# Kernel tuning notes

Hardware: AMD Instinct MI355X
Metric: run time of the kernel (lower is better)

## Reference

```python
import jax, jax.numpy as jnp
import numpy as np

H, T, D = 16, 4096, 64
N_SEQ = 8  # packed sequences -> cu_seqlens has N_SEQ+1 entries


def setup_inputs() -> dict:
    key = jax.random.key(0)
    kq, kk, kv, kc = jax.random.split(key, 4)
    q = jax.random.normal(kq, (1, H, T, D), dtype=jnp.float32)
    k = jax.random.normal(kk, (1, H, T, D), dtype=jnp.float32)
    v = jax.random.normal(kv, (1, H, T, D), dtype=jnp.float32)
    # cu_seqlens: monotonically increasing offsets, starts at 0, ends at T
    interior = jnp.sort(jax.random.randint(kc, (N_SEQ - 1,), 1, T, dtype=jnp.int32))
    cu_seqlens = jnp.concatenate([
        jnp.zeros((1,), jnp.int32), interior, jnp.full((1,), T, jnp.int32)
    ])
    return {"q": q, "k": k, "v": v, "cu_seqlens": cu_seqlens}


def reference(q, k, v, cu_seqlens):
    # Faithful to flash_attn_varlen_func(..., causal=False) on packed sequences:
    # non-causal attention restricted block-diagonally to each segment.
    scale = 1.0 / jnp.sqrt(jnp.asarray(D, q.dtype))
    # segment id for every token position
    pos = jnp.arange(T)
    seg = jnp.searchsorted(cu_seqlens[1:], pos, side="right")  # [T]
    mask = seg[:, None] == seg[None, :]                         # [T, T] block-diagonal
    # scores: [1, H, T, T]
    scores = jnp.einsum("bhqd,bhkd->bhqk", q, k) * scale
    neg = jnp.asarray(jnp.finfo(scores.dtype).min, scores.dtype)
    scores = jnp.where(mask[None, None], scores, neg)
    attn = jax.nn.softmax(scores, axis=-1)
    out = jnp.einsum("bhqk,bhkd->bhqd", attn, v)  # [1, H, T, D]
    return out
```

## Files before the change

### kernel.cpp

```cpp
#include <hip/hip_runtime.h>

#define HH 16
#define TT 4096
#define DD 64

typedef __attribute__((ext_vector_type(2))) __fp16 half2r;
typedef __attribute__((ext_vector_type(4))) _Float16 half4;
typedef __attribute__((ext_vector_type(8))) _Float16 half8;
typedef __attribute__((ext_vector_type(4))) float float4v;

__global__ __launch_bounds__(256, 4) void pa_fwd(
    const float* __restrict__ qg, const float* __restrict__ kg,
    const float* __restrict__ vg, const int* __restrict__ cu,
    float* __restrict__ outg)
{
    __shared__ __align__(16) _Float16 Kl[2][64 * 64];
    __shared__ __align__(16) _Float16 Vl[2][64 * 64];

    const int tid  = threadIdx.x;
    const int lane = tid & 63;
    const int wave = tid >> 6;
    const int lr   = lane & 15;
    const int lg   = lane >> 4;

    const int bswz = ((int)blockIdx.x & 7) * 128 + ((int)blockIdx.x >> 3);
    const int h    = bswz >> 6;
    const int qblk = (bswz & 63) << 6;
    const int q    = qblk + wave * 16 + lr;

    int s = 0;
    while (cu[s + 1] <= q) ++s;
    const int lo = cu[s], hi = cu[s + 1];

    int sb = 0;
    while (cu[sb + 1] <= qblk) ++sb;
    const int blo = cu[sb];
    while (cu[sb + 1] <= qblk + 63) ++sb;
    const int bhi = cu[sb + 1];

    const int wlo = __shfl(lo, 0);
    const int whi = __shfl(hi, 15);
    const int mlo = __shfl(lo, 15);
    const int mhi = __shfl(hi, 0);

    const float qscale = 0.125f * 1.44269504088896f;
    const float* qrow = qg + ((size_t)h * TT + q) * DD;
    half8 qf8[2];
#pragma unroll
    for (int ds = 0; ds < 2; ++ds) {
        const float* qp = qrow + ds * 32 + lg * 8;
        float4v a = *(const float4v*)qp;
        float4v b = *(const float4v*)(qp + 4);
        half2r p0 = __builtin_amdgcn_cvt_pkrtz(a[0] * qscale, a[1] * qscale);
        half2r p1 = __builtin_amdgcn_cvt_pkrtz(a[2] * qscale, a[3] * qscale);
        half2r p2 = __builtin_amdgcn_cvt_pkrtz(b[0] * qscale, b[1] * qscale);
        half2r p3 = __builtin_amdgcn_cvt_pkrtz(b[2] * qscale, b[3] * qscale);
        qf8[ds][0] = (_Float16)p0[0]; qf8[ds][1] = (_Float16)p0[1];
        qf8[ds][2] = (_Float16)p1[0]; qf8[ds][3] = (_Float16)p1[1];
        qf8[ds][4] = (_Float16)p2[0]; qf8[ds][5] = (_Float16)p2[1];
        qf8[ds][6] = (_Float16)p3[0]; qf8[ds][7] = (_Float16)p3[1];
    }

    const float* kh_ = kg + (size_t)h * TT * DD;
    const float* vh_ = vg + (size_t)h * TT * DD;

    const int srow = tid >> 2;
    const int sc   = tid & 3;
    const unsigned kwrA = (unsigned)(srow * 128 + (((2 * sc)     ^ (srow & 7)) << 4));
    const unsigned kwrB = (unsigned)(srow * 128 + (((2 * sc + 1) ^ (srow & 7)) << 4));
    const int vd2 = tid & 31;
    const int vko = tid >> 5;
    const int vslot = vko ^ (vd2 & 7);
    const int vhb   = (vd2 >> 3) & 1;
    const unsigned vwA0 = (unsigned)(vd2 * 128 + vslot * 16 + 8 * vhb);
    const unsigned vwA1 = (unsigned)(vd2 * 128 + vslot * 16 + 8 * (1 ^ vhb));
    const unsigned vwB0 = vwA0 + 32 * 128;
    const unsigned vwB1 = vwA1 + 32 * 128;

    const unsigned kb0 = (unsigned)(lr * 128 + (((lg)     ^ (lr & 7)) << 4));
    const unsigned kb1 = (unsigned)(lr * 128 + (((4 + lg) ^ (lr & 7)) << 4));
    unsigned vrb[4];
#pragma unroll
    for (int t = 0; t < 4; ++t)
        vrb[t] = (unsigned)(lr * 128 + (((2 * t + (lg >> 1)) ^ (lr & 7)) << 4) +
                            (((lg & 1) ^ ((lr >> 3) & 1)) << 3));

    half4 onesv;
    onesv[0] = onesv[1] = onesv[2] = onesv[3] = (_Float16)1.0f;

    float4v kq[4];
    float vvA[8], vvB[8];
    const int t0k = blo & ~63;
    const float4v* kp = (const float4v*)(kh_ + (size_t)(t0k + srow) * DD + sc * 16);
    const float*   vp = vh_ + (size_t)(t0k + vko * 8) * DD + vd2;

#define ISSUE()                                                                \
    {                                                                          \
        kq[0] = kp[0]; kq[1] = kp[1]; kq[2] = kp[2]; kq[3] = kp[3];            \
        kp += (64 * DD) / 4;                                                   \
        _Pragma("unroll")                                                      \
        for (int c = 0; c < 8; ++c) {                                          \
            vvA[c] = vp[c * DD];                                               \
            vvB[c] = vp[c * DD + 32];                                          \
        }                                                                      \
        vp += 64 * DD;                                                         \
    }

    ISSUE();

    float4v acc[4];
#pragma unroll
    for (int dt = 0; dt < 4; ++dt) acc[dt] = (float4v){0.f, 0.f, 0.f, 0.f};
    float4v acc_l = (float4v){0.f, 0.f, 0.f, 0.f};
    float m_run = -1e30f;

    int cur = 0;
    for (int kt = t0k; kt < bhi; kt += 64) {
        {
            char* Kb = (char*)Kl[cur];
            char* Vb = (char*)Vl[cur];
            half8 hk0, hk1;
#pragma unroll
            for (int i = 0; i < 2; ++i) {
                half2r a = __builtin_amdgcn_cvt_pkrtz(kq[i][0], kq[i][1]);
                half2r b = __builtin_amdgcn_cvt_pkrtz(kq[i][2], kq[i][3]);
                hk0[4 * i + 0] = (_Float16)a[0]; hk0[4 * i + 1] = (_Float16)a[1];
                hk0[4 * i + 2] = (_Float16)b[0]; hk0[4 * i + 3] = (_Float16)b[1];
                half2r c2 = __builtin_amdgcn_cvt_pkrtz(kq[2 + i][0], kq[2 + i][1]);
                half2r d2 = __builtin_amdgcn_cvt_pkrtz(kq[2 + i][2], kq[2 + i][3]);
                hk1[4 * i + 0] = (_Float16)c2[0]; hk1[4 * i + 1] = (_Float16)c2[1];
                hk1[4 * i + 2] = (_Float16)d2[0]; hk1[4 * i + 3] = (_Float16)d2[1];
            }
            *(half8*)(Kb + kwrA) = hk0;
            *(half8*)(Kb + kwrB) = hk1;

            half4 uA0, uA1, uB0, uB1;
            {
                half2r a = __builtin_amdgcn_cvt_pkrtz(vvA[0], vvA[1]);
                half2r b = __builtin_amdgcn_cvt_pkrtz(vvA[2], vvA[3]);
                uA0[0] = (_Float16)a[0]; uA0[1] = (_Float16)a[1];
                uA0[2] = (_Float16)b[0]; uA0[3] = (_Float16)b[1];
                half2r c2 = __builtin_amdgcn_cvt_pkrtz(vvA[4], vvA[5]);
                half2r d2 = __builtin_amdgcn_cvt_pkrtz(vvA[6], vvA[7]);
                uA1[0] = (_Float16)c2[0]; uA1[1] = (_Float16)c2[1];
                uA1[2] = (_Float16)d2[0]; uA1[3] = (_Float16)d2[1];
                half2r e = __builtin_amdgcn_cvt_pkrtz(vvB[0], vvB[1]);
                half2r f = __builtin_amdgcn_cvt_pkrtz(vvB[2], vvB[3]);
                uB0[0] = (_Float16)e[0]; uB0[1] = (_Float16)e[1];
                uB0[2] = (_Float16)f[0]; uB0[3] = (_Float16)f[1];
                half2r g = __builtin_amdgcn_cvt_pkrtz(vvB[4], vvB[5]);
                half2r k2 = __builtin_amdgcn_cvt_pkrtz(vvB[6], vvB[7]);
                uB1[0] = (_Float16)g[0]; uB1[1] = (_Float16)g[1];
                uB1[2] = (_Float16)k2[0]; uB1[3] = (_Float16)k2[1];
            }
            *(half4*)(Vb + vwA0) = uA0;
            *(half4*)(Vb + vwA1) = uA1;
            *(half4*)(Vb + vwB0) = uB0;
            *(half4*)(Vb + vwB1) = uB1;
        }
        __syncthreads();

        if (kt + 64 < bhi) ISSUE();

        if (!(kt + 64 <= wlo || kt >= whi)) {
            const char* Kb = (const char*)Kl[cur];
            const char* Vb = (const char*)Vl[cur];

            float st[4][4];
            const bool fullv = (kt >= mlo) && (kt + 64 <= mhi);
            __builtin_amdgcn_s_setprio(1);
#pragma unroll
            for (int t = 0; t < 4; ++t) {
                float4v sa = (float4v){0.f, 0.f, 0.f, 0.f};
                half8 kf0 = *(const half8*)(Kb + kb0 + t * 2048);
                half8 kf1 = *(const half8*)(Kb + kb1 + t * 2048);
                sa = __builtin_amdgcn_mfma_f32_16x16x32_f16(kf0, qf8[0], sa, 0, 0, 0);
                sa = __builtin_amdgcn_mfma_f32_16x16x32_f16(kf1, qf8[1], sa, 0, 0, 0);
                if (fullv) {
#pragma unroll
                    for (int j = 0; j < 4; ++j) st[t][j] = sa[j];
                } else {
#pragma unroll
                    for (int j = 0; j < 4; ++j) {
                        const int key = kt + t * 16 + lg * 4 + j;
                        st[t][j] = (key >= lo && key < hi) ? sa[j] : -1e30f;
                    }
                }
            }
            __builtin_amdgcn_s_setprio(0);

            half4 vf01[2][4];
#pragma unroll
            for (int t = 0; t < 2; ++t)
#pragma unroll
                for (int dt = 0; dt < 4; ++dt)
                    vf01[t][dt] = *(const half4*)(Vb + vrb[t] + dt * 2048);

            float lmax = fmaxf(fmaxf(st[0][0], st[0][1]), fmaxf(st[0][2], st[0][3]));
            lmax = fmaxf(lmax, fmaxf(fmaxf(st[1][0], st[1][1]), fmaxf(st[1][2], st[1][3])));
            lmax = fmaxf(lmax, fmaxf(fmaxf(st[2][0], st[2][1]), fmaxf(st[2][2], st[2][3])));
            lmax = fmaxf(lmax, fmaxf(fmaxf(st[3][0], st[3][1]), fmaxf(st[3][2], st[3][3])));

            if (__any(lmax > m_run + 11.54f)) {
                float tx = fmaxf(lmax, __shfl_xor(lmax, 16));
                tx = fmaxf(tx, __shfl_xor(tx, 32));
                const float mn = fmaxf(m_run, tx);
                const float a  = exp2f(m_run - mn);
#pragma unroll
                for (int dt = 0; dt < 4; ++dt)
#pragma unroll
                    for (int j = 0; j < 4; ++j) acc[dt][j] *= a;
#pragma unroll
                for (int j = 0; j < 4; ++j) acc_l[j] *= a;
                m_run = mn;
            }

            half4 pb[4];
#pragma unroll
            for (int t = 0; t < 4; ++t) {
                float e0 = exp2f(st[t][0] - m_run);
                float e1 = exp2f(st[t][1] - m_run);
                float e2 = exp2f(st[t][2] - m_run);
                float e3 = exp2f(st[t][3] - m_run);
                half2r a = __builtin_amdgcn_cvt_pkrtz(e0, e1);
                half2r b = __builtin_amdgcn_cvt_pkrtz(e2, e3);
                pb[t][0] = (_Float16)a[0]; pb[t][1] = (_Float16)a[1];
                pb[t][2] = (_Float16)b[0]; pb[t][3] = (_Float16)b[1];
            }

            __builtin_amdgcn_s_setprio(1);
#pragma unroll
            for (int t = 0; t < 2; ++t) {
#pragma unroll
                for (int dt = 0; dt < 4; ++dt)
                    acc[dt] = __builtin_amdgcn_mfma_f32_16x16x16f16(vf01[t][dt], pb[t], acc[dt], 0, 0, 0);
                acc_l = __builtin_amdgcn_mfma_f32_16x16x16f16(onesv, pb[t], acc_l, 0, 0, 0);
            }
#pragma unroll
            for (int t = 2; t < 4; ++t) {
#pragma unroll
                for (int dt = 0; dt < 4; ++dt) {
                    half4 vf = *(const half4*)(Vb + vrb[t] + dt * 2048);
                    acc[dt] = __builtin_amdgcn_mfma_f32_16x16x16f16(vf, pb[t], acc[dt], 0, 0, 0);
                }
                acc_l = __builtin_amdgcn_mfma_f32_16x16x16f16(onesv, pb[t], acc_l, 0, 0, 0);
            }
            __builtin_amdgcn_s_setprio(0);
        }
        cur ^= 1;
    }

    const float inv = 1.0f / acc_l[0];
    float* orow = outg + ((size_t)h * TT + q) * DD;
#pragma unroll
    for (int dt = 0; dt < 4; ++dt) {
        float4v o;
#pragma unroll
        for (int j = 0; j < 4; ++j) o[j] = acc[dt][j] * inv;
        *(float4v*)(orow + dt * 16 + lg * 4) = o;
    }
#undef ISSUE
}

extern "C" void kernel_launch(void* const* d_in, const int* in_sizes, int n_in,
                              void* d_out, int out_size, void* d_ws, size_t ws_size,
                              hipStream_t stream) {
    const float* q  = (const float*)d_in[0];
    const float* k  = (const float*)d_in[1];
    const float* v  = (const float*)d_in[2];
    const int*   cu = (const int*)d_in[3];
    float* out = (float*)d_out;

    dim3 grid(HH * (TT / 64));
    dim3 block(256);
    hipLaunchKernelGGL(pa_fwd, grid, block, 0, stream, q, k, v, cu, out);
}
```

Baseline: 81.31 us.

## Split key range across two wave groups per block and merge softmax partials

Doubles the block to 512 threads, forming two groups of four waves. The groups take alternating 64-key tiles over the same 64 queries, each keeping its own double-buffered LDS tiles. At the end, group 1 writes its accumulator, running max and row sum to shared memory, and group 0 merges them with a log-sum-exp rescale before writing the output. This shortens the serial key loop per wave, at the cost of doubled LDS use, which may lower occupancy, plus an extra merge and barriers.

```diff
diff --git a/kernel.cpp b/kernel.cpp
--- a/kernel.cpp
+++ b/kernel.cpp
@@ -9,24 +9,27 @@
 typedef __attribute__((ext_vector_type(8))) _Float16 half8;
 typedef __attribute__((ext_vector_type(4))) float float4v;
 
-__global__ __launch_bounds__(256, 4) void pa_fwd(
+__global__ __launch_bounds__(512, 4) void pa_fwd(
     const float* __restrict__ qg, const float* __restrict__ kg,
     const float* __restrict__ vg, const int* __restrict__ cu,
     float* __restrict__ outg)
 {
-    __shared__ __align__(16) _Float16 Kl[2][64 * 64];
-    __shared__ __align__(16) _Float16 Vl[2][64 * 64];
-
-    const int tid  = threadIdx.x;
-    const int lane = tid & 63;
-    const int wave = tid >> 6;
-    const int lr   = lane & 15;
-    const int lg   = lane >> 4;
+    __shared__ __align__(16) _Float16 Kl[2][2][64 * 64];
+    __shared__ __align__(16) _Float16 Vl[2][2][64 * 64];
+
+    const int tid   = threadIdx.x;
+    const int lane  = tid & 63;
+    const int wavei = tid >> 6;
+    const int grp   = wavei >> 2;
+    const int wv    = wavei & 3;
+    const int gtid  = tid & 255;
+    const int lr    = lane & 15;
+    const int lg    = lane >> 4;
 
     const int bswz = ((int)blockIdx.x & 7) * 128 + ((int)blockIdx.x >> 3);
     const int h    = bswz >> 6;
     const int qblk = (bswz & 63) << 6;
-    const int q    = qblk + wave * 16 + lr;
+    const int q    = qblk + wv * 16 + lr;
 
     int s = 0;
     while (cu[s + 1] <= q) ++s;
@@ -64,12 +67,12 @@
     const float* kh_ = kg + (size_t)h * TT * DD;
     const float* vh_ = vg + (size_t)h * TT * DD;
 
-    const int srow = tid >> 2;
-    const int sc   = tid & 3;
+    const int srow = gtid >> 2;
+    const int sc   = gtid & 3;
     const unsigned kwrA = (unsigned)(srow * 128 + (((2 * sc)     ^ (srow & 7)) << 4));
     const unsigned kwrB = (unsigned)(srow * 128 + (((2 * sc + 1) ^ (srow & 7)) << 4));
-    const int vd2 = tid & 31;
-    const int vko = tid >> 5;
+    const int vd2 = gtid & 31;
+    const int vko = gtid >> 5;
     const int vslot = vko ^ (vd2 & 7);
     const int vhb   = (vd2 >> 3) & 1;
     const unsigned vwA0 = (unsigned)(vd2 * 128 + vslot * 16 + 8 * vhb);
@@ -91,22 +94,23 @@
     float4v kq[4];
     float vvA[8], vvB[8];
     const int t0k = blo & ~63;
-    const float4v* kp = (const float4v*)(kh_ + (size_t)(t0k + srow) * DD + sc * 16);
-    const float*   vp = vh_ + (size_t)(t0k + vko * 8) * DD + vd2;
+    const int t0g = t0k + (grp << 6);
+    const float4v* kp = (const float4v*)(kh_ + (size_t)(t0g + srow) * DD + sc * 16);
+    const float*   vp = vh_ + (size_t)(t0g + vko * 8) * DD + vd2;
 
 #define ISSUE()                                                                \
     {                                                                          \
         kq[0] = kp[0]; kq[1] = kp[1]; kq[2] = kp[2]; kq[3] = kp[3];            \
-        kp += (64 * DD) / 4;                                                   \
+        kp += (128 * DD) / 4;                                                  \
         _Pragma("unroll")                                                      \
         for (int c = 0; c < 8; ++c) {                                          \
             vvA[c] = vp[c * DD];                                               \
             vvB[c] = vp[c * DD + 32];                                          \
         }                                                                      \
-        vp += 64 * DD;                                                         \
-    }
-
-    ISSUE();
+        vp += 128 * DD;                                                        \
+    }
+
+    if (t0g < bhi) ISSUE();
 
     float4v acc[4];
 #pragma unroll
@@ -115,10 +119,13 @@
     float m_run = -1e30f;
 
     int cur = 0;
-    for (int kt = t0k; kt < bhi; kt += 64) {
-        {
-            char* Kb = (char*)Kl[cur];
-            char* Vb = (char*)Vl[cur];
+    for (int kt = t0k; kt < bhi; kt += 128) {
+        const int ktg = kt + (grp << 6);
+        const bool vg = ktg < bhi;
+
+        if (vg) {
+            char* Kb = (char*)Kl[grp][cur];
+            char* Vb = (char*)Vl[grp][cur];
             half8 hk0, hk1;
 #pragma unroll
             for (int i = 0; i < 2; ++i) {
@@ -160,14 +167,14 @@
         }
         __syncthreads();
 
-        if (kt + 64 < bhi) ISSUE();
-
-        if (!(kt + 64 <= wlo || kt >= whi)) {
-            const char* Kb = (const char*)Kl[cur];
-            const char* Vb = (const char*)Vl[cur];
+        if (vg && ktg + 128 < bhi) ISSUE();
+
+        if (vg && !(ktg + 64 <= wlo || ktg >= whi)) {
+            const char* Kb = (const char*)Kl[grp][cur];
+            const char* Vb = (const char*)Vl[grp][cur];
 
             float st[4][4];
-            const bool fullv = (kt >= mlo) && (kt + 64 <= mhi);
+            const bool fullv = (ktg >= mlo) && (ktg + 64 <= mhi);
             __builtin_amdgcn_s_setprio(1);
 #pragma unroll
             for (int t = 0; t < 4; ++t) {
@@ -182,7 +189,7 @@
                 } else {
 #pragma unroll
                     for (int j = 0; j < 4; ++j) {
-                        const int key = kt + t * 16 + lg * 4 + j;
+                        const int key = ktg + t * 16 + lg * 4 + j;
                         st[t][j] = (key >= lo && key < hi) ? sa[j] : -1e30f;
                     }
                 }
@@ -250,14 +257,37 @@
         cur ^= 1;
     }
 
-    const float inv = 1.0f / acc_l[0];
-    float* orow = outg + ((size_t)h * TT + q) * DD;
-#pragma unroll
-    for (int dt = 0; dt < 4; ++dt) {
-        float4v o;
-#pragma unroll
-        for (int j = 0; j < 4; ++j) o[j] = acc[dt][j] * inv;
-        *(float4v*)(orow + dt * 16 + lg * 4) = o;
+    float* mb = (float*)&Kl[0][0][0];
+    float* ml = (float*)&Vl[0][0][0];
+
+    __syncthreads();
+    if (grp == 1) {
+        const int r = wv * 16 + lr;
+#pragma unroll
+        for (int dt = 0; dt < 4; ++dt)
+            *(float4v*)(mb + r * 64 + dt * 16 + lg * 4) = acc[dt];
+        if (lg == 0) { ml[r] = m_run; ml[64 + r] = acc_l[0]; }
+    }
+    __syncthreads();
+    if (grp == 0) {
+        const int r  = wv * 16 + lr;
+        const float mB = ml[r];
+        const float lB = ml[64 + r];
+        const float M  = fmaxf(m_run, mB);
+        const float eA = exp2f(m_run - M);
+        const float eB = exp2f(mB - M);
+        const float inv = 1.0f / (eA * acc_l[0] + eB * lB);
+
+        float* orow = outg + ((size_t)h * TT + q) * DD;
+#pragma unroll
+        for (int dt = 0; dt < 4; ++dt) {
+            float4v aB = *(const float4v*)(mb + r * 64 + dt * 16 + lg * 4);
+            float4v o;
+#pragma unroll
+            for (int j = 0; j < 4; ++j)
+                o[j] = (eA * acc[dt][j] + eB * aB[j]) * inv;
+            *(float4v*)(orow + dt * 16 + lg * 4) = o;
+        }
     }
 #undef ISSUE
 }
@@ -272,6 +302,6 @@
     float* out = (float*)d_out;
 
     dim3 grid(HH * (TT / 64));
-    dim3 block(256);
+    dim3 block(512);
     hipLaunchKernelGGL(pa_fwd, grid, block, 0, stream, q, k, v, cu, out);
 }
```

Result: slower. 90.16 us (+10.9%).
